# Performance work log

Measured on AMD Instinct MI355X. Metric: run time of the kernel, lower is better.

Reference implementation:

```python
import jax, jax.numpy as jnp
import numpy as np

EPS = 1e-8


def setup_inputs() -> dict:
    key0 = jax.random.key(0)
    k1, k2, k3 = jax.random.split(key0, 3)
    B, Q, K, H, D = 8, 16, 65536, 1, 64
    query = jax.random.normal(k1, (B, Q, H, D), dtype=jnp.float32)
    key = jax.random.normal(k2, (B, K, H, D), dtype=jnp.float32)
    value = jax.random.normal(k3, (B, K, H, D), dtype=jnp.float32)
    return {"query": query, "key": key, "value": value}


def reference(query, key, value):
    # query: [B, Q, H, D]; key/value: [B, K, H, D]
    qk_features = query.shape[-1]
    q = query * (1.0 / np.sqrt(qk_features)).astype(np.float32)
    # scores: [B, H, Q, K]
    attn = jnp.einsum('bqhd,bkhd->bhqk', q, key)
    # inverted attention: softmax over the QUERY axis (-2)
    attn = jax.nn.softmax(attn, axis=-2)
    # renormalize over keys ('mean' norm_type)
    normalizer = jnp.sum(attn, axis=-1, keepdims=True) + EPS
    attn_n = attn / normalizer
    # updates: [B, Q, H, D]
    updates = jnp.einsum('bhqk,bkhd->bqhd', attn_n, value)
    # num_heads == 1 -> squeeze head dim: [B, Q, D]
    output = jnp.squeeze(updates, axis=-2)
    return (output, attn)
```

## Files before the change

### kernel.cpp

```cpp
#include <hip/hip_runtime.h>

#define KTOT 65536
#define QN 16
#define DN 64
#define BN 8
#define TILE 256

#define QS_OFF 0
#define R0_OFF 1024
#define R1_OFF 5120
#define SMEM_FLOATS 9216

typedef float f2v __attribute__((ext_vector_type(2)));
typedef float f4v __attribute__((ext_vector_type(4)));

#define PK_MUL(d, a, b) asm("v_pk_mul_f32 %0, %1, %2"     : "=v"(d) : "v"(a), "v"(b))
#define PK_FMA(d, a, b) asm("v_pk_fma_f32 %0, %1, %2, %0" : "+v"(d) : "v"(a), "v"(b))

__device__ __forceinline__ void gload_lds16(const float* g, float* l)
{
    __builtin_amdgcn_global_load_lds(
        (const __attribute__((address_space(1))) void*)g,
        (__attribute__((address_space(3))) void*)l, 16, 0, 0);
}

#define WAIT_VM(N)  asm volatile("s_waitcnt vmcnt(" #N ")" ::: "memory")
#define LGKM0()     asm volatile("s_waitcnt lgkmcnt(0)" ::: "memory")

#define STAGE_WV(RX, kb4, qo4)                                                      \
    {                                                                               \
        _Pragma("unroll")                                                           \
        for (int j = 0; j < 4; ++j) {                                               \
            const int r_ = (wv << 6) + (j << 4) + (lane >> 2);                      \
            const int p_ = (lane & 3) ^ ((r_ >> 1) & 3);                            \
            gload_lds16((const float*)((kb4) + r_ * 16 + (qo4) + p_),               \
                        (float*)(((float4*)&smem[RX]) + ((wv << 8) + (j << 6) + lane))); \
        }                                                                           \
    }

#define DOT_Q(qt, RX)                                                               \
    {                                                                               \
        __builtin_amdgcn_s_setprio(1);                                              \
        f4v kvv[4];                                                                 \
        _Pragma("unroll")                                                           \
        for (int cc = 0; cc < 4; ++cc)                                              \
            kvv[cc] = ((const f4v*)&smem[RX])[tid * 4 + (cc ^ fr)];                 \
        _Pragma("unroll")                                                           \
        for (int q = 0; q < QN; ++q) {                                              \
            const f4v qv0 = *(const f4v*)&smem[QS_OFF + q * DN + (qt) * 16 + 0];    \
            const f4v qv1 = *(const f4v*)&smem[QS_OFF + q * DN + (qt) * 16 + 4];    \
            const f4v qv2 = *(const f4v*)&smem[QS_OFF + q * DN + (qt) * 16 + 8];    \
            const f4v qv3 = *(const f4v*)&smem[QS_OFF + q * DN + (qt) * 16 + 12];   \
            f2v t;                                                                  \
            PK_MUL(t, kvv[0].xy, qv0.xy);                                           \
            PK_FMA(t, kvv[0].zw, qv0.zw);                                           \
            PK_FMA(t, kvv[1].xy, qv1.xy);                                           \
            PK_FMA(t, kvv[1].zw, qv1.zw);                                           \
            PK_FMA(t, kvv[2].xy, qv2.xy);                                           \
            PK_FMA(t, kvv[2].zw, qv2.zw);                                           \
            PK_FMA(t, kvv[3].xy, qv3.xy);                                           \
            PK_FMA(t, kvv[3].zw, qv3.zw);                                           \
            s[q] += t.x + t.y;                                                      \
        }                                                                           \
        __builtin_amdgcn_s_setprio(0);                                              \
    }

__global__ __launch_bounds__(256, 3) void fused_attn(
    const float* __restrict__ query, const float* __restrict__ key,
    const float* __restrict__ value, float* __restrict__ attn,
    float* __restrict__ upart, int NCH, int ntiles)
{
    __shared__ float smem[SMEM_FLOATS];
    const int b    = blockIdx.y;
    const int c    = blockIdx.x;
    const int tid  = threadIdx.x;
    const int wv   = tid >> 6;
    const int lane = tid & 63;
    const int chunk = ntiles * TILE;
    const int fr   = (tid >> 1) & 3;
    const int AW   = R1_OFF + wv * (QN * 64);

    {
        float4 qv = reinterpret_cast<const float4*>(query + (size_t)b * QN * DN)[tid];
        qv.x *= 0.125f; qv.y *= 0.125f; qv.z *= 0.125f; qv.w *= 0.125f;
        reinterpret_cast<float4*>(&smem[QS_OFF])[tid] = qv;
    }
    __syncthreads();

    {
        const float4* kb4 = reinterpret_cast<const float4*>(
            key + ((size_t)b * KTOT + c * chunk) * DN);
        STAGE_WV(R0_OFF, kb4, 0);
        STAGE_WV(R1_OFF, kb4, 4);
    }

    float U[QN];
    #pragma unroll
    for (int q = 0; q < QN; ++q) U[q] = 0.f;

    for (int t = 0; t < ntiles; ++t) {
        const int krow0 = c * chunk + t * TILE;
        const float4* kb4  = reinterpret_cast<const float4*>(
            key + ((size_t)b * KTOT + krow0) * DN);
        const float4* kb4n = kb4 + TILE * 16;
        const float*  vptr = value + ((size_t)b * KTOT + krow0 + wv * 64) * DN + lane;

        float s[QN];
        #pragma unroll
        for (int q = 0; q < QN; ++q) s[q] = 0.f;

        WAIT_VM(4);
        DOT_Q(0, R0_OFF);
        LGKM0(); STAGE_WV(R0_OFF, kb4, 8);

        WAIT_VM(4);
        DOT_Q(1, R1_OFF);
        LGKM0(); STAGE_WV(R1_OFF, kb4, 12);

        WAIT_VM(4);
        DOT_Q(2, R0_OFF);

        f2v va2[4];
        #pragma unroll
        for (int i = 0; i < 4; ++i) {
            va2[i].x = vptr[(size_t)(2 * i) * DN];
            va2[i].y = vptr[(size_t)(2 * i + 1) * DN];
        }
        WAIT_VM(8);
        DOT_Q(3, R1_OFF);

        float m = s[0];
        #pragma unroll
        for (int q = 1; q < QN; ++q) m = fmaxf(m, s[q]);
        float sum = 0.f;
        #pragma unroll
        for (int q = 0; q < QN; ++q) { s[q] = __expf(s[q] - m); sum += s[q]; }
        const float inv = 1.0f / sum;
        {
            float* ab = attn + (size_t)b * QN * KTOT + krow0 + tid;
            #pragma unroll
            for (int q = 0; q < QN; ++q) {
                const float a = s[q] * inv;
                __builtin_nontemporal_store(a, ab + (size_t)q * KTOT);
                smem[AW + q * 64 + lane] = a;
            }
        }

        #pragma unroll 1
        for (int kk = 0; kk < 64; kk += 8) {
            f2v vb2[4];
            const int nxt = kk + 8;
            if (nxt < 64) {
                #pragma unroll
                for (int i = 0; i < 4; ++i) {
                    vb2[i].x = vptr[(size_t)(nxt + 2 * i) * DN];
                    vb2[i].y = vptr[(size_t)(nxt + 2 * i + 1) * DN];
                }
            }
            __builtin_amdgcn_s_setprio(1);
            #pragma unroll
            for (int q = 0; q < QN; ++q) {
                const f4v av0 = *(const f4v*)&smem[AW + q * 64 + kk];
                const f4v av1 = *(const f4v*)&smem[AW + q * 64 + kk + 4];
                f2v t;
                PK_MUL(t, av0.xy, va2[0]);
                PK_FMA(t, av0.zw, va2[1]);
                PK_FMA(t, av1.xy, va2[2]);
                PK_FMA(t, av1.zw, va2[3]);
                U[q] += t.x + t.y;
            }
            __builtin_amdgcn_s_setprio(0);
            #pragma unroll
            for (int i = 0; i < 4; ++i) va2[i] = vb2[i];
        }

        if (t + 1 < ntiles) {
            LGKM0();
            STAGE_WV(R0_OFF, kb4n, 0);
            STAGE_WV(R1_OFF, kb4n, 4);
        }
    }

    __syncthreads();
    #pragma unroll
    for (int q = 0; q < QN; ++q)
        smem[R0_OFF + (wv * QN + q) * DN + lane] = U[q];
    __syncthreads();

    {
        const int q = tid >> 4, d0 = (tid & 15) * 4;
        const float4 r0 = *reinterpret_cast<const float4*>(&smem[R0_OFF + (0 * QN + q) * DN + d0]);
        const float4 r1 = *reinterpret_cast<const float4*>(&smem[R0_OFF + (1 * QN + q) * DN + d0]);
        const float4 r2 = *reinterpret_cast<const float4*>(&smem[R0_OFF + (2 * QN + q) * DN + d0]);
        const float4 r3 = *reinterpret_cast<const float4*>(&smem[R0_OFF + (3 * QN + q) * DN + d0]);
        float4 rs;
        rs.x = r0.x + r1.x + r2.x + r3.x;
        rs.y = r0.y + r1.y + r2.y + r3.y;
        rs.z = r0.z + r1.z + r2.z + r3.z;
        rs.w = r0.w + r1.w + r2.w + r3.w;
        *reinterpret_cast<float4*>(
            &upart[(((size_t)b * NCH + c) * QN + q) * DN + d0]) = rs;
    }
}

__global__ __launch_bounds__(256) void k_norm(
    const float* __restrict__ attn, float* __restrict__ normp2)
{
    const int b = blockIdx.x, q = blockIdx.y, z = blockIdx.z;
    const int tid = threadIdx.x;
    const float4* ap = reinterpret_cast<const float4*>(
        attn + ((size_t)b * QN + q) * KTOT + (size_t)z * 8192);
    float nv = 0.f;
    #pragma unroll
    for (int i = 0; i < 8; ++i) {
        const float4 a = ap[i * 256 + tid];
        nv += (a.x + a.y) + (a.z + a.w);
    }
    #pragma unroll
    for (int off = 1; off < 64; off <<= 1) nv += __shfl_xor(nv, off, 64);
    __shared__ float red[4];
    if ((tid & 63) == 0) red[tid >> 6] = nv;
    __syncthreads();
    if (tid == 0)
        normp2[((b * QN + q) << 3) + z] = red[0] + red[1] + red[2] + red[3];
}

__global__ __launch_bounds__(256) void k3_fin(
    const float* __restrict__ upart, const float* __restrict__ normp2,
    float* __restrict__ out, int NCH)
{
    const int b = blockIdx.x, q = blockIdx.y;
    const int tid = threadIdx.x;
    const int wv = tid >> 6, lane = tid & 63;

    float acc = 0.f;
    for (int c = wv; c < NCH; c += 4)
        acc += upart[(((size_t)b * NCH + c) * QN + q) * DN + lane];
    __shared__ float ured[4][DN];
    ured[wv][lane] = acc;
    __syncthreads();

    if (tid < DN) {
        float n = 0.f;
        #pragma unroll
        for (int i = 0; i < 8; ++i)
            n += normp2[((b * QN + q) << 3) + i];
        const float inv = 1.0f / (n + 1e-8f);
        const float u   = ured[0][tid] + ured[1][tid] + ured[2][tid] + ured[3][tid];
        out[((size_t)b * QN + q) * DN + tid] = u * inv;
    }
}

extern "C" void kernel_launch(void* const* d_in, const int* in_sizes, int n_in,
                              void* d_out, int out_size, void* d_ws, size_t ws_size,
                              hipStream_t stream)
{
    const float* query = (const float*)d_in[0];
    const float* key   = (const float*)d_in[1];
    const float* value = (const float*)d_in[2];

    float* out  = (float*)d_out;
    float* attn = (float*)d_out + (size_t)BN * QN * DN;

    int NCH = 128;
    while (NCH > 8 &&
           ((size_t)BN * NCH * QN * DN + BN * QN * 8) * 4 > ws_size) NCH >>= 1;
    const int ntiles = (KTOT / NCH) / TILE;

    float* upart  = (float*)d_ws;
    float* normp2 = (float*)d_ws + (size_t)BN * NCH * QN * DN;

    fused_attn<<<dim3(NCH, BN), 256, 0, stream>>>(query, key, value, attn,
                                                  upart, NCH, ntiles);
    k_norm   <<<dim3(BN, QN, 8), 256, 0, stream>>>(attn, normp2);
    k3_fin   <<<dim3(BN, QN),    256, 0, stream>>>(upart, normp2, out, NCH);
}
```

Baseline: 77.21 us.

## Triple-buffer key staging in LDS with rotating buffer offsets

Replaces the two fixed LDS key staging regions with three rotating buffers, so two quarter-tiles stay in flight ahead of the dot-product consumer instead of one. The wait counts and the staging schedule are reordered so the next tile's loads are issued earlier, hiding more global-load latency. LDS use per block grows from about 36KB to 52KB. That may cut occupancy below the three blocks per CU requested in launch bounds, and the rotating offsets become runtime values rather than constants.

```diff
diff --git a/kernel.cpp b/kernel.cpp
--- a/kernel.cpp
+++ b/kernel.cpp
@@ -7,9 +7,10 @@
 #define TILE 256
 
 #define QS_OFF 0
-#define R0_OFF 1024
-#define R1_OFF 5120
-#define SMEM_FLOATS 9216
+#define RA_OFF 1024
+#define RB_OFF 5120
+#define RC_OFF 9216
+#define SMEM_FLOATS 13312
 
 typedef float f2v __attribute__((ext_vector_type(2)));
 typedef float f4v __attribute__((ext_vector_type(4)));
@@ -78,7 +79,6 @@
     const int lane = tid & 63;
     const int chunk = ntiles * TILE;
     const int fr   = (tid >> 1) & 3;
-    const int AW   = R1_OFF + wv * (QN * 64);
 
     {
         float4 qv = reinterpret_cast<const float4*>(query + (size_t)b * QN * DN)[tid];
@@ -87,11 +87,14 @@
     }
     __syncthreads();
 
+    int ra = RA_OFF, rb = RB_OFF, rc = RC_OFF;
+
     {
         const float4* kb4 = reinterpret_cast<const float4*>(
             key + ((size_t)b * KTOT + c * chunk) * DN);
-        STAGE_WV(R0_OFF, kb4, 0);
-        STAGE_WV(R1_OFF, kb4, 4);
+        STAGE_WV(ra, kb4, 0);
+        STAGE_WV(rb, kb4, 4);
+        STAGE_WV(rc, kb4, 8);
     }
 
     float U[QN];
@@ -104,21 +107,21 @@
             key + ((size_t)b * KTOT + krow0) * DN);
         const float4* kb4n = kb4 + TILE * 16;
         const float*  vptr = value + ((size_t)b * KTOT + krow0 + wv * 64) * DN + lane;
+        const int AW = ra + wv * (QN * 64);
 
         float s[QN];
         #pragma unroll
         for (int q = 0; q < QN; ++q) s[q] = 0.f;
 
+        WAIT_VM(8);
+        DOT_Q(0, ra);
+        LGKM0(); STAGE_WV(ra, kb4, 12);
+
+        WAIT_VM(8);
+        DOT_Q(1, rb);
+
         WAIT_VM(4);
-        DOT_Q(0, R0_OFF);
-        LGKM0(); STAGE_WV(R0_OFF, kb4, 8);
-
-        WAIT_VM(4);
-        DOT_Q(1, R1_OFF);
-        LGKM0(); STAGE_WV(R1_OFF, kb4, 12);
-
-        WAIT_VM(4);
-        DOT_Q(2, R0_OFF);
+        DOT_Q(2, rc);
 
         f2v va2[4];
         #pragma unroll
@@ -127,7 +130,7 @@
             va2[i].y = vptr[(size_t)(2 * i + 1) * DN];
         }
         WAIT_VM(8);
-        DOT_Q(3, R1_OFF);
+        DOT_Q(3, ra);
 
         float m = s[0];
         #pragma unroll
@@ -176,23 +179,26 @@
 
         if (t + 1 < ntiles) {
             LGKM0();
-            STAGE_WV(R0_OFF, kb4n, 0);
-            STAGE_WV(R1_OFF, kb4n, 4);
-        }
+            STAGE_WV(rb, kb4n, 0);
+            STAGE_WV(rc, kb4n, 4);
+            STAGE_WV(ra, kb4n, 8);
+        }
+
+        const int tmp = ra; ra = rb; rb = rc; rc = tmp;
     }
 
     __syncthreads();
     #pragma unroll
     for (int q = 0; q < QN; ++q)
-        smem[R0_OFF + (wv * QN + q) * DN + lane] = U[q];
+        smem[RA_OFF + (wv * QN + q) * DN + lane] = U[q];
     __syncthreads();
 
     {
         const int q = tid >> 4, d0 = (tid & 15) * 4;
-        const float4 r0 = *reinterpret_cast<const float4*>(&smem[R0_OFF + (0 * QN + q) * DN + d0]);
-        const float4 r1 = *reinterpret_cast<const float4*>(&smem[R0_OFF + (1 * QN + q) * DN + d0]);
-        const float4 r2 = *reinterpret_cast<const float4*>(&smem[R0_OFF + (2 * QN + q) * DN + d0]);
-        const float4 r3 = *reinterpret_cast<const float4*>(&smem[R0_OFF + (3 * QN + q) * DN + d0]);
+        const float4 r0 = *reinterpret_cast<const float4*>(&smem[RA_OFF + (0 * QN + q) * DN + d0]);
+        const float4 r1 = *reinterpret_cast<const float4*>(&smem[RA_OFF + (1 * QN + q) * DN + d0]);
+        const float4 r2 = *reinterpret_cast<const float4*>(&smem[RA_OFF + (2 * QN + q) * DN + d0]);
+        const float4 r3 = *reinterpret_cast<const float4*>(&smem[RA_OFF + (3 * QN + q) * DN + d0]);
         float4 rs;
         rs.x = r0.x + r1.x + r2.x + r3.x;
         rs.y = r0.y + r1.y + r2.y + r3.y;
```

New measurement: 95.11 us. +23.2%, slower.
